# Performance work log

Measured on AMD Instinct MI355X. Metric: run time of the kernel, lower is better.

## Reference

```python
import jax, jax.numpy as jnp
import numpy as np

N_PTS = 20000  # points per cloud


def setup_inputs() -> dict:
    key = jax.random.key(0)
    k1, k2 = jax.random.split(key)
    preds = jax.random.normal(k1, (N_PTS, 3), dtype=jnp.float32)
    gts = jax.random.normal(k2, (1, N_PTS, 3), dtype=jnp.float32)
    return {"preds": preds, "gts": gts}


def reference(preds, gts):
    # x = gts: [B, Nx, 3]; y = preds.unsqueeze(0): [1, Ny, 3] (B must be 1 for bmm)
    y = preds[None]                                   # [1, Ny, 3]
    x = gts                                           # [1, Nx, 3]
    xx = jnp.sum(x * x, axis=-1)                      # [1, Nx]  (diag of x x^T)
    yy = jnp.sum(y * y, axis=-1)                      # [1, Ny]
    zz = jnp.einsum('bnd,bmd->bnm', x, y)             # [1, Nx, Ny]
    P = xx[:, :, None] + yy[:, None, :] - 2.0 * zz    # [1, Nx, Ny] squared dists
    dist1 = jnp.min(P, axis=1)                        # [1, Ny] min over gts points
    dist2 = jnp.min(P, axis=2)                        # [1, Nx] min over pred points
    idx1 = jnp.argmin(P, axis=1)                      # [1, Ny]
    idx2 = jnp.argmin(P, axis=2)                      # [1, Nx]
    return dist1, dist2, idx1, idx2
```

## Files before the change

kernel.cpp:

```cpp
#include <hip/hip_runtime.h>

#define N_PTS  20000
#define NG     128
#define NC     (NG * NG)
#define GMIN   (-6.0f)
#define GINV   (NG / 12.0f)
#define MARGIN 5e-4f
#define SSTRIDE (N_PTS / 64)
#define QB79   79

__device__ __forceinline__ float np_self_dot(float x, float y, float z) {
    return __fadd_rn(__fadd_rn(__fmul_rn(x, x), __fmul_rn(y, y)),
                     __fmul_rn(z, z));
}
__device__ __forceinline__ unsigned ordmap(float f) {
    unsigned b = __float_as_uint(f);
    return (b & 0x80000000u) ? ~b : (b | 0x80000000u);
}
__device__ __forceinline__ float invord(unsigned h) {
    return __uint_as_float((h & 0x80000000u) ? (h ^ 0x80000000u) : ~h);
}
__device__ __forceinline__ int cellC(float v) {
    int c = (int)((v - GMIN) * GINV);
    return c < 0 ? 0 : (c > NG - 1 ? NG - 1 : c);
}
__device__ __forceinline__ unsigned long long wave_min_u64(unsigned long long k) {
    #pragma unroll
    for (int m = 1; m < 64; m <<= 1) {
        unsigned long long o = __shfl_xor(k, m, 64);
        k = (o < k) ? o : k;
    }
    return k;
}

__global__ __launch_bounds__(256) void k_hist(
    const float* __restrict__ preds, const float* __restrict__ gts,
    int* __restrict__ cursor)
{
    int t = blockIdx.x * 256 + threadIdx.x;
    if (t >= 2 * N_PTS) return;
    int cl = t / N_PTS, i = t - cl * N_PTS;
    const float* src = cl ? gts : preds;
    int cell = cellC(src[i*3+0]) * NG + cellC(src[i*3+1]);
    atomicAdd(&cursor[cl * NC + cell], 1);
}

__global__ __launch_bounds__(1024) void k_scan(
    int* __restrict__ cursor, int* __restrict__ bstart)
{
    __shared__ int wsum[16];
    __shared__ int wpre[16];
    int cl = blockIdx.x, t = threadIdx.x;
    int wave = t >> 6, lane = t & 63;

    int base = cl * NC + t * 16;
    const int4* c4 = (const int4*)(cursor + base);
    int4 a = c4[0], b = c4[1], c = c4[2], d = c4[3];
    int v[16] = { a.x, a.y, a.z, a.w, b.x, b.y, b.z, b.w,
                  c.x, c.y, c.z, c.w, d.x, d.y, d.z, d.w };
    int s = 0;
    #pragma unroll
    for (int i = 0; i < 16; ++i) s += v[i];

    int ps = s;
    #pragma unroll
    for (int m = 1; m < 64; m <<= 1) {
        int o = __shfl_up(ps, m, 64);
        if (lane >= m) ps += o;
    }
    if (lane == 63) wsum[wave] = ps;
    __syncthreads();
    if (t < 16) {
        int x = wsum[t];
        int px = x;
        #pragma unroll
        for (int m = 1; m < 16; m <<= 1) {
            int o = __shfl_up(px, m, 16);
            if ((t & 15) >= m) px += o;
        }
        wpre[t] = px - x;
    }
    __syncthreads();

    int run = wpre[wave] + (ps - s);
    #pragma unroll
    for (int i = 0; i < 16; ++i) {
        bstart[cl * (NC + 1) + t * 16 + i] = run;
        cursor[base + i] = run;
        run += v[i];
    }
    if (t == 1023) bstart[cl * (NC + 1) + NC] = run;
}

__global__ __launch_bounds__(256) void k_scatter(
    const float* __restrict__ preds, const float* __restrict__ gts,
    int* __restrict__ cursor, float4* __restrict__ sorted)
{
    int t = blockIdx.x * 256 + threadIdx.x;
    if (t >= 2 * N_PTS) return;
    int cl = t / N_PTS, i = t - cl * N_PTS;
    const float* src = cl ? gts : preds;
    float x = src[i*3+0], y = src[i*3+1], z = src[i*3+2];
    int cell = cellC(x) * NG + cellC(y);
    int pos = atomicAdd(&cursor[cl * NC + cell], 1);
    sorted[(size_t)cl * N_PTS + pos] = make_float4(x, y, z, __int_as_float(i));
}

__global__ __launch_bounds__(64) void k_main(
    const float4* __restrict__ sorted, const int* __restrict__ bstart,
    float* __restrict__ out)
{
    int wid  = blockIdx.x;
    int lane = threadIdx.x;
    int dir  = wid / N_PTS;
    int qpos = wid - dir * N_PTS;
    int rcl  = 1 - dir;

    const float4* rs = sorted + (size_t)rcl * N_PTS;
    const int*    cs = bstart + rcl * (NC + 1);

    float4 samp = rs[lane * SSTRIDE];
    float4 qv   = sorted[(size_t)dir * N_PTS + qpos];
    int    origq = __float_as_int(qv.w);
    float qx = qv.x, qy = qv.y, qz = qv.z;
    float sq = np_self_dot(qx, qy, qz);

    unsigned long long key = ~0ULL;

#define EVAL(r)                                                            \
    {   float sr = np_self_dot((r).x, (r).y, (r).z);                       \
        float zz = __fadd_rn(__fadd_rn(__fmul_rn(qx, (r).x),               \
                                       __fmul_rn(qy, (r).y)),              \
                             __fmul_rn(qz, (r).z));                        \
        float P  = __fsub_rn(__fadd_rn(sq, sr), __fadd_rn(zz, zz));        \
        unsigned long long kk =                                            \
            ((unsigned long long)ordmap(P) << 32) | __float_as_uint((r).w);\
        key = (kk < key) ? kk : key; }

#define STREAM(LO, HI)                                                     \
    {   int p = (LO) + lane;                                               \
        for (; p + 192 < (HI); p += 256) {                                 \
            float4 r0 = rs[p],       r1 = rs[p + 64];                      \
            float4 r2 = rs[p + 128], r3 = rs[p + 192];                     \
            EVAL(r0) EVAL(r1) EVAL(r2) EVAL(r3)                            \
        }                                                                  \
        for (; p + 64 < (HI); p += 128) {                                  \
            float4 r0 = rs[p], r1 = rs[p + 64];                            \
            EVAL(r0) EVAL(r1)                                              \
        }                                                                  \
        if (p < (HI)) { float4 r0 = rs[p]; EVAL(r0) }                      \
    }

    int cx = cellC(qx), cy = cellC(qy);
    int sxL = cx > 0 ? cx - 1 : 0, sxR = cx < NG-1 ? cx + 1 : NG-1;
    int syL = cy > 0 ? cy - 1 : 0, syR = cy < NG-1 ? cy + 1 : NG-1;
    int slo = cs[sxL * NG + syL];
    int shi = cs[sxR * NG + syR + 1];
    STREAM(slo, shi)
    EVAL(samp)

    key = wave_min_u64(key);
    float W = sqrtf(invord((unsigned)(key >> 32)) + MARGIN);
    int txL = cellC(qx - W), txR = cellC(qx + W);
    int tyL = cellC(qy - W), tyR = cellC(qy + W);
    int lo2 = cs[txL * NG + tyL];
    int hi2 = cs[txR * NG + tyR + 1];
    if (lo2 < slo) STREAM(lo2, slo)
    if (hi2 > shi) STREAM(shi, hi2)
    key = wave_min_u64(key);
#undef STREAM
#undef EVAL

    if (lane == 0) {
        out[dir * N_PTS + origq]       = invord((unsigned)(key >> 32));
        out[(2 + dir) * N_PTS + origq] = (float)(unsigned)(key & 0xFFFFFFFFu);
    }
}

__device__ __forceinline__ float np_pair(float sq, float sr,
                                         float qx, float qy, float qz,
                                         float rx, float ry, float rz) {
    float zz = __fadd_rn(__fadd_rn(__fmul_rn(qx, rx), __fmul_rn(qy, ry)),
                         __fmul_rn(qz, rz));
    return __fsub_rn(__fadd_rn(sq, sr), __fadd_rn(zz, zz));
}

__global__ __launch_bounds__(256) void chamfer_direct_kernel(
    const float* __restrict__ preds, const float* __restrict__ gts,
    float* __restrict__ out)
{
    __shared__ float4 spts[256];
    int bid = blockIdx.x;
    int dir = bid / QB79;
    int qb  = bid - dir * QB79;
    int q   = qb * 256 + threadIdx.x;

    const float* qpts = (dir == 0) ? preds : gts;
    const float* rpts = (dir == 0) ? gts   : preds;

    int qc = (q < N_PTS) ? q : (N_PTS - 1);
    float qx = qpts[qc*3+0], qy = qpts[qc*3+1], qz = qpts[qc*3+2];
    float sq = np_self_dot(qx, qy, qz);
    float best = 3.4e38f;
    int   bidx = 0;

    for (int t = 0; t < N_PTS; t += 256) {
        int cnt = min(256, N_PTS - t);
        __syncthreads();
        if ((int)threadIdx.x < cnt) {
            int j = t + threadIdx.x;
            float rx = rpts[j*3+0], ry = rpts[j*3+1], rz = rpts[j*3+2];
            spts[threadIdx.x] = make_float4(rx, ry, rz, np_self_dot(rx, ry, rz));
        }
        __syncthreads();
        for (int k = 0; k < cnt; ++k) {
            float4 r = spts[k];
            float d = np_pair(sq, r.w, qx, qy, qz, r.x, r.y, r.z);
            if (d < best) { best = d; bidx = t + k; }
        }
    }
    if (q < N_PTS) {
        out[dir * N_PTS + q]       = best;
        out[(2 + dir) * N_PTS + q] = (float)bidx;
    }
}

extern "C" void kernel_launch(void* const* d_in, const int* in_sizes, int n_in,
                              void* d_out, int out_size, void* d_ws, size_t ws_size,
                              hipStream_t stream) {
    const float* preds = (const float*)d_in[0];
    const float* gts   = (const float*)d_in[1];
    float* out = (float*)d_out;

    char* w = (char*)d_ws;
    size_t sorted_b = (size_t)2 * N_PTS * sizeof(float4);
    size_t bstart_b = (size_t)2 * (NC + 1) * sizeof(int);
    size_t cursor_b = (size_t)2 * NC * sizeof(int);
    size_t need = sorted_b + bstart_b + cursor_b;

    if (ws_size >= need) {
        float4* sorted = (float4*)w;
        int* bstart = (int*)(w + sorted_b);
        int* cursor = (int*)(w + sorted_b + bstart_b);

        hipMemsetAsync(cursor, 0, cursor_b, stream);
        k_hist<<<(2 * N_PTS + 255) / 256, 256, 0, stream>>>(preds, gts, cursor);
        k_scan<<<2, 1024, 0, stream>>>(cursor, bstart);
        k_scatter<<<(2 * N_PTS + 255) / 256, 256, 0, stream>>>(
            preds, gts, cursor, sorted);
        k_main<<<2 * N_PTS, 64, 0, stream>>>(sorted, bstart, out);
    } else {
        chamfer_direct_kernel<<<2 * QB79, 256, 0, stream>>>(preds, gts, out);
    }
}
```

Baseline: 126.6 us.

## Stream only per-row cell spans in grid NN search instead of contiguous ranges

The nearest-neighbor query now loads per-x-row cell boundaries in parallel across lanes and streams only the y-window span within each row, instead of scanning the whole contiguous sorted range from the first to the last cell. The second pass is skipped when the search window already lies inside the initial 3x3 neighborhood, and otherwise re-scans the full window row by row. A software-prefetched single-element loop flattens the three row spans so the lanes stay busy. This is meant to cut the many irrelevant points evaluated between rows, at the cost of extra shuffles, index arithmetic and re-evaluating points already covered by the first pass.

```diff
diff --git a/kernel.cpp b/kernel.cpp
--- a/kernel.cpp
+++ b/kernel.cpp
@@ -31,6 +31,37 @@
         k = (o < k) ? o : k;
     }
     return k;
+}
+
+#define EVAL(r)                                                            \
+    {   float sr = np_self_dot((r).x, (r).y, (r).z);                       \
+        float zz = __fadd_rn(__fadd_rn(__fmul_rn(qx, (r).x),               \
+                                       __fmul_rn(qy, (r).y)),              \
+                             __fmul_rn(qz, (r).z));                        \
+        float P  = __fsub_rn(__fadd_rn(sq, sr), __fadd_rn(zz, zz));        \
+        unsigned long long kk =                                            \
+            ((unsigned long long)ordmap(P) << 32) | __float_as_uint((r).w);\
+        key = (kk < key) ? kk : key; }
+
+__device__ __forceinline__ void stream3(
+    const float4* __restrict__ rs, int lane,
+    int lo0, int c0, int lo1, int c1, int lo2, int c2,
+    float qx, float qy, float qz, float sq, unsigned long long& key)
+{
+    int s01 = c0 + c1, tot = s01 + c2;
+    int t = lane;
+    if (t < tot) {
+        int p = t < c0 ? lo0 + t : t < s01 ? lo1 + (t - c0) : lo2 + (t - s01);
+        float4 rc = rs[p];
+        for (t += 64; t < tot; t += 64) {
+            int pn = t < c0 ? lo0 + t : t < s01 ? lo1 + (t - c0)
+                                                : lo2 + (t - s01);
+            float4 rn = rs[pn];
+            EVAL(rc)
+            rc = rn;
+        }
+        EVAL(rc)
+    }
 }
 
 __global__ __launch_bounds__(256) void k_hist(
@@ -126,50 +157,50 @@
     float sq = np_self_dot(qx, qy, qz);
 
     unsigned long long key = ~0ULL;
-
-#define EVAL(r)                                                            \
-    {   float sr = np_self_dot((r).x, (r).y, (r).z);                       \
-        float zz = __fadd_rn(__fadd_rn(__fmul_rn(qx, (r).x),               \
-                                       __fmul_rn(qy, (r).y)),              \
-                             __fmul_rn(qz, (r).z));                        \
-        float P  = __fsub_rn(__fadd_rn(sq, sr), __fadd_rn(zz, zz));        \
-        unsigned long long kk =                                            \
-            ((unsigned long long)ordmap(P) << 32) | __float_as_uint((r).w);\
-        key = (kk < key) ? kk : key; }
-
-#define STREAM(LO, HI)                                                     \
-    {   int p = (LO) + lane;                                               \
-        for (; p + 192 < (HI); p += 256) {                                 \
-            float4 r0 = rs[p],       r1 = rs[p + 64];                      \
-            float4 r2 = rs[p + 128], r3 = rs[p + 192];                     \
-            EVAL(r0) EVAL(r1) EVAL(r2) EVAL(r3)                            \
-        }                                                                  \
-        for (; p + 64 < (HI); p += 128) {                                  \
-            float4 r0 = rs[p], r1 = rs[p + 64];                            \
-            EVAL(r0) EVAL(r1)                                              \
-        }                                                                  \
-        if (p < (HI)) { float4 r0 = rs[p]; EVAL(r0) }                      \
-    }
+    int l31 = lane & 31;
 
     int cx = cellC(qx), cy = cellC(qy);
     int sxL = cx > 0 ? cx - 1 : 0, sxR = cx < NG-1 ? cx + 1 : NG-1;
     int syL = cy > 0 ? cy - 1 : 0, syR = cy < NG-1 ? cy + 1 : NG-1;
-    int slo = cs[sxL * NG + syL];
-    int shi = cs[sxR * NG + syR + 1];
-    STREAM(slo, shi)
+    int nrs  = sxR - sxL + 1;
+    int xrS  = sxL + (l31 < nrs ? l31 : nrs - 1);
+    int colS = (lane < 32) ? syL : (syR + 1);
+    int bndS = cs[xrS * NG + colS];
+    int lo0 = __shfl(bndS, 0, 64), hi0 = __shfl(bndS, 32, 64);
+    int lo1 = __shfl(bndS, 1, 64), hi1 = __shfl(bndS, 33, 64);
+    int lo2 = __shfl(bndS, 2, 64), hi2 = __shfl(bndS, 34, 64);
+    int c0 = hi0 - lo0;
+    int c1 = nrs > 1 ? hi1 - lo1 : 0;
+    int c2 = nrs > 2 ? hi2 - lo2 : 0;
+    stream3(rs, lane, lo0, c0, lo1, c1, lo2, c2, qx, qy, qz, sq, key);
     EVAL(samp)
 
     key = wave_min_u64(key);
     float W = sqrtf(invord((unsigned)(key >> 32)) + MARGIN);
     int txL = cellC(qx - W), txR = cellC(qx + W);
     int tyL = cellC(qy - W), tyR = cellC(qy + W);
-    int lo2 = cs[txL * NG + tyL];
-    int hi2 = cs[txR * NG + tyR + 1];
-    if (lo2 < slo) STREAM(lo2, slo)
-    if (hi2 > shi) STREAM(shi, hi2)
-    key = wave_min_u64(key);
-#undef STREAM
-#undef EVAL
+    if (!(txL >= sxL && txR <= sxR && tyL >= syL && tyR <= syR)) {
+        int R = txR - txL + 1;
+        for (int g = 0; g < R; g += 32) {
+            int rows = R - g; if (rows > 32) rows = 32;
+            int xr2  = txL + g + (l31 < rows ? l31 : rows - 1);
+            int col2 = (lane < 32) ? tyL : (tyR + 1);
+            int b2 = cs[xr2 * NG + col2];
+            for (int r0 = 0; r0 < rows; r0 += 3) {
+                int i1 = r0 + 1 < rows ? r0 + 1 : rows - 1;
+                int i2 = r0 + 2 < rows ? r0 + 2 : rows - 1;
+                int L0 = __shfl(b2, r0, 64), H0 = __shfl(b2, 32 + r0, 64);
+                int L1 = __shfl(b2, i1, 64), H1 = __shfl(b2, 32 + i1, 64);
+                int L2 = __shfl(b2, i2, 64), H2 = __shfl(b2, 32 + i2, 64);
+                int d0 = H0 - L0;
+                int d1 = (r0 + 1 < rows) ? H1 - L1 : 0;
+                int d2 = (r0 + 2 < rows) ? H2 - L2 : 0;
+                stream3(rs, lane, L0, d0, L1, d1, L2, d2,
+                        qx, qy, qz, sq, key);
+            }
+        }
+        key = wave_min_u64(key);
+    }
 
     if (lane == 0) {
         out[dir * N_PTS + origq]       = invord((unsigned)(key >> 32));
```

New measurement: 122.4 us. 3.3% less time.

## Process two queries per wave and scan exact cell rectangles per row

Applied to the files above, without the earlier changes.

Each wave now handles two adjacent sorted query points and shares every loaded reference point between them, halving the block count. Instead of streaming the contiguous range from the first to last cell (which spans whole x-rows of the grid), it reads per-row segment bounds for the exact cell rectangle and packs three rows at a time across lanes. The second pass is skipped when the refined window lies inside the first rectangle. In exchange, the union rectangle for two queries can be larger than either query needs, and the per-row bookkeeping adds shuffles and index arithmetic.

```diff
diff --git a/kernel.cpp b/kernel.cpp
--- a/kernel.cpp
+++ b/kernel.cpp
@@ -32,6 +32,27 @@
     }
     return k;
 }
+__device__ __forceinline__ int imin2(int a, int b) { return a < b ? a : b; }
+__device__ __forceinline__ int imax2(int a, int b) { return a > b ? a : b; }
+
+#define EVAL2(r)                                                           \
+    {   float rx = (r).x, ry = (r).y, rz = (r).z;                          \
+        float sr = np_self_dot(rx, ry, rz);                                \
+        unsigned ridx = __float_as_uint((r).w);                            \
+        float za = __fadd_rn(__fadd_rn(__fmul_rn(qax, rx),                 \
+                                       __fmul_rn(qay, ry)),                \
+                             __fmul_rn(qaz, rz));                          \
+        float Pa = __fsub_rn(__fadd_rn(sqa, sr), __fadd_rn(za, za));       \
+        unsigned long long kka =                                           \
+            ((unsigned long long)ordmap(Pa) << 32) | ridx;                 \
+        ka = (kka < ka) ? kka : ka;                                        \
+        float zb = __fadd_rn(__fadd_rn(__fmul_rn(qbx, rx),                 \
+                                       __fmul_rn(qby, ry)),                \
+                             __fmul_rn(qbz, rz));                          \
+        float Pb = __fsub_rn(__fadd_rn(sqb, sr), __fadd_rn(zb, zb));       \
+        unsigned long long kkb =                                           \
+            ((unsigned long long)ordmap(Pb) << 32) | ridx;                 \
+        kb = (kkb < kb) ? kkb : kb; }
 
 __global__ __launch_bounds__(256) void k_hist(
     const float* __restrict__ preds, const float* __restrict__ gts,
@@ -112,68 +133,90 @@
 {
     int wid  = blockIdx.x;
     int lane = threadIdx.x;
-    int dir  = wid / N_PTS;
-    int qpos = wid - dir * N_PTS;
+    int q0   = wid * 2;
+    int dir  = q0 / N_PTS;
+    int qp0  = q0 - dir * N_PTS;
     int rcl  = 1 - dir;
 
     const float4* rs = sorted + (size_t)rcl * N_PTS;
     const int*    cs = bstart + rcl * (NC + 1);
 
     float4 samp = rs[lane * SSTRIDE];
-    float4 qv   = sorted[(size_t)dir * N_PTS + qpos];
-    int    origq = __float_as_int(qv.w);
-    float qx = qv.x, qy = qv.y, qz = qv.z;
-    float sq = np_self_dot(qx, qy, qz);
-
-    unsigned long long key = ~0ULL;
-
-#define EVAL(r)                                                            \
-    {   float sr = np_self_dot((r).x, (r).y, (r).z);                       \
-        float zz = __fadd_rn(__fadd_rn(__fmul_rn(qx, (r).x),               \
-                                       __fmul_rn(qy, (r).y)),              \
-                             __fmul_rn(qz, (r).z));                        \
-        float P  = __fsub_rn(__fadd_rn(sq, sr), __fadd_rn(zz, zz));        \
-        unsigned long long kk =                                            \
-            ((unsigned long long)ordmap(P) << 32) | __float_as_uint((r).w);\
-        key = (kk < key) ? kk : key; }
-
-#define STREAM(LO, HI)                                                     \
-    {   int p = (LO) + lane;                                               \
-        for (; p + 192 < (HI); p += 256) {                                 \
-            float4 r0 = rs[p],       r1 = rs[p + 64];                      \
-            float4 r2 = rs[p + 128], r3 = rs[p + 192];                     \
-            EVAL(r0) EVAL(r1) EVAL(r2) EVAL(r3)                            \
+    float4 qva  = sorted[(size_t)dir * N_PTS + qp0];
+    float4 qvb  = sorted[(size_t)dir * N_PTS + qp0 + 1];
+    int oa = __float_as_int(qva.w), ob = __float_as_int(qvb.w);
+    float qax = qva.x, qay = qva.y, qaz = qva.z;
+    float qbx = qvb.x, qby = qvb.y, qbz = qvb.z;
+    float sqa = np_self_dot(qax, qay, qaz);
+    float sqb = np_self_dot(qbx, qby, qbz);
+
+    unsigned long long ka = ~0ULL, kb = ~0ULL;
+    int l31 = lane & 31;
+
+#define SCAN_RECT(xL, xR, yL, yR)                                          \
+    {   int R = (xR) - (xL) + 1;                                           \
+        for (int g = 0; g < R; g += 32) {                                  \
+            int rows = R - g; if (rows > 32) rows = 32;                    \
+            int xr  = (xL) + g + (l31 < rows ? l31 : rows - 1);            \
+            int col = (lane < 32) ? (yL) : ((yR) + 1);                     \
+            int b2 = cs[xr * NG + col];                                    \
+            for (int r0 = 0; r0 < rows; r0 += 3) {                         \
+                int i1 = r0 + 1 < rows ? r0 + 1 : rows - 1;                \
+                int i2 = r0 + 2 < rows ? r0 + 2 : rows - 1;                \
+                int L0 = __shfl(b2, r0, 64), H0 = __shfl(b2, 32 + r0, 64); \
+                int L1 = __shfl(b2, i1, 64), H1 = __shfl(b2, 32 + i1, 64); \
+                int L2 = __shfl(b2, i2, 64), H2 = __shfl(b2, 32 + i2, 64); \
+                int d0 = H0 - L0;                                          \
+                int d1 = (r0 + 1 < rows) ? H1 - L1 : 0;                    \
+                int d2 = (r0 + 2 < rows) ? H2 - L2 : 0;                    \
+                int s01 = d0 + d1, tot = s01 + d2;                         \
+                int t = lane;                                              \
+                if (t < tot) {                                             \
+                    int p = t < d0 ? L0 + t : t < s01 ? L1 + (t - d0)      \
+                                                      : L2 + (t - s01);   \
+                    float4 rc = rs[p];                                     \
+                    for (t += 64; t < tot; t += 64) {                      \
+                        int pn = t < d0 ? L0 + t : t < s01 ? L1 + (t - d0) \
+                                                           : L2 + (t - s01);\
+                        float4 rn = rs[pn];                                \
+                        EVAL2(rc)                                          \
+                        rc = rn;                                           \
+                    }                                                      \
+                    EVAL2(rc)                                              \
+                }                                                          \
+            }                                                              \
         }                                                                  \
-        for (; p + 64 < (HI); p += 128) {                                  \
-            float4 r0 = rs[p], r1 = rs[p + 64];                            \
-            EVAL(r0) EVAL(r1)                                              \
-        }                                                                  \
-        if (p < (HI)) { float4 r0 = rs[p]; EVAL(r0) }                      \
-    }
-
-    int cx = cellC(qx), cy = cellC(qy);
-    int sxL = cx > 0 ? cx - 1 : 0, sxR = cx < NG-1 ? cx + 1 : NG-1;
-    int syL = cy > 0 ? cy - 1 : 0, syR = cy < NG-1 ? cy + 1 : NG-1;
-    int slo = cs[sxL * NG + syL];
-    int shi = cs[sxR * NG + syR + 1];
-    STREAM(slo, shi)
-    EVAL(samp)
-
-    key = wave_min_u64(key);
-    float W = sqrtf(invord((unsigned)(key >> 32)) + MARGIN);
-    int txL = cellC(qx - W), txR = cellC(qx + W);
-    int tyL = cellC(qy - W), tyR = cellC(qy + W);
-    int lo2 = cs[txL * NG + tyL];
-    int hi2 = cs[txR * NG + tyR + 1];
-    if (lo2 < slo) STREAM(lo2, slo)
-    if (hi2 > shi) STREAM(shi, hi2)
-    key = wave_min_u64(key);
-#undef STREAM
-#undef EVAL
+    }
+
+    int cxa = cellC(qax), cya = cellC(qay);
+    int cxb = cellC(qbx), cyb = cellC(qby);
+    int sxL = imax2(imin2(cxa, cxb) - 1, 0);
+    int sxR = imin2(imax2(cxa, cxb) + 1, NG - 1);
+    int syL = imax2(imin2(cya, cyb) - 1, 0);
+    int syR = imin2(imax2(cya, cyb) + 1, NG - 1);
+    SCAN_RECT(sxL, sxR, syL, syR)
+    EVAL2(samp)
+
+    ka = wave_min_u64(ka);
+    kb = wave_min_u64(kb);
+    float Wa = sqrtf(invord((unsigned)(ka >> 32)) + MARGIN);
+    float Wb = sqrtf(invord((unsigned)(kb >> 32)) + MARGIN);
+    int txL = imin2(cellC(qax - Wa), cellC(qbx - Wb));
+    int txR = imax2(cellC(qax + Wa), cellC(qbx + Wb));
+    int tyL = imin2(cellC(qay - Wa), cellC(qby - Wb));
+    int tyR = imax2(cellC(qay + Wa), cellC(qby + Wb));
+    if (!(txL >= sxL && txR <= sxR && tyL >= syL && tyR <= syR)) {
+        SCAN_RECT(txL, txR, tyL, tyR)
+        ka = wave_min_u64(ka);
+        kb = wave_min_u64(kb);
+    }
+#undef SCAN_RECT
 
     if (lane == 0) {
-        out[dir * N_PTS + origq]       = invord((unsigned)(key >> 32));
-        out[(2 + dir) * N_PTS + origq] = (float)(unsigned)(key & 0xFFFFFFFFu);
+        out[dir * N_PTS + oa]       = invord((unsigned)(ka >> 32));
+        out[(2 + dir) * N_PTS + oa] = (float)(unsigned)(ka & 0xFFFFFFFFu);
+        out[dir * N_PTS + ob]       = invord((unsigned)(kb >> 32));
+        out[(2 + dir) * N_PTS + ob] = (float)(unsigned)(kb & 0xFFFFFFFFu);
     }
 }
 
@@ -248,7 +291,7 @@
         k_scan<<<2, 1024, 0, stream>>>(cursor, bstart);
         k_scatter<<<(2 * N_PTS + 255) / 256, 256, 0, stream>>>(
             preds, gts, cursor, sorted);
-        k_main<<<2 * N_PTS, 64, 0, stream>>>(sorted, bstart, out);
+        k_main<<<N_PTS, 64, 0, stream>>>(sorted, bstart, out);
     } else {
         chamfer_direct_kernel<<<2 * QB79, 256, 0, stream>>>(preds, gts, out);
     }
```

Result: slower. 135.8 us (+7.3%).

## Scan grid rectangles row-by-row instead of contiguous index range

Applied to the files above, without the earlier changes.

Replaces streaming the whole contiguous sorted-index span (which covers entire rows of cells between the corner cells) with a per-row rectangle scan that fetches row start and end offsets via shuffles and processes three rows per batch. The initial search window grows from 3x3 to 5x5 cells, and the second pass is skipped when the refined window fits inside the first rectangle. This is meant to cut the many wasted point evaluations from full-row spans, in exchange for more index arithmetic, shuffles and a possibly rescanned overlap in the second pass.

```diff
diff --git a/kernel.cpp b/kernel.cpp
--- a/kernel.cpp
+++ b/kernel.cpp
@@ -32,6 +32,16 @@
     }
     return k;
 }
+
+#define EVAL(r)                                                            \
+    {   float sr = np_self_dot((r).x, (r).y, (r).z);                       \
+        float zz = __fadd_rn(__fadd_rn(__fmul_rn(qx, (r).x),               \
+                                       __fmul_rn(qy, (r).y)),              \
+                             __fmul_rn(qz, (r).z));                        \
+        float P  = __fsub_rn(__fadd_rn(sq, sr), __fadd_rn(zz, zz));        \
+        unsigned long long kk =                                            \
+            ((unsigned long long)ordmap(P) << 32) | __float_as_uint((r).w);\
+        key = (kk < key) ? kk : key; }
 
 __global__ __launch_bounds__(256) void k_hist(
     const float* __restrict__ preds, const float* __restrict__ gts,
@@ -126,50 +136,58 @@
     float sq = np_self_dot(qx, qy, qz);
 
     unsigned long long key = ~0ULL;
-
-#define EVAL(r)                                                            \
-    {   float sr = np_self_dot((r).x, (r).y, (r).z);                       \
-        float zz = __fadd_rn(__fadd_rn(__fmul_rn(qx, (r).x),               \
-                                       __fmul_rn(qy, (r).y)),              \
-                             __fmul_rn(qz, (r).z));                        \
-        float P  = __fsub_rn(__fadd_rn(sq, sr), __fadd_rn(zz, zz));        \
-        unsigned long long kk =                                            \
-            ((unsigned long long)ordmap(P) << 32) | __float_as_uint((r).w);\
-        key = (kk < key) ? kk : key; }
-
-#define STREAM(LO, HI)                                                     \
-    {   int p = (LO) + lane;                                               \
-        for (; p + 192 < (HI); p += 256) {                                 \
-            float4 r0 = rs[p],       r1 = rs[p + 64];                      \
-            float4 r2 = rs[p + 128], r3 = rs[p + 192];                     \
-            EVAL(r0) EVAL(r1) EVAL(r2) EVAL(r3)                            \
+    int l31 = lane & 31;
+
+#define SCAN_RECT(xL, xR, yL, yR)                                          \
+    {   int R = (xR) - (xL) + 1;                                           \
+        for (int g = 0; g < R; g += 32) {                                  \
+            int rows = R - g; if (rows > 32) rows = 32;                    \
+            int xr  = (xL) + g + (l31 < rows ? l31 : rows - 1);            \
+            int col = (lane < 32) ? (yL) : ((yR) + 1);                     \
+            int b2 = cs[xr * NG + col];                                    \
+            for (int r0 = 0; r0 < rows; r0 += 3) {                         \
+                int i1 = r0 + 1 < rows ? r0 + 1 : rows - 1;                \
+                int i2 = r0 + 2 < rows ? r0 + 2 : rows - 1;                \
+                int L0 = __shfl(b2, r0, 64), H0 = __shfl(b2, 32 + r0, 64); \
+                int L1 = __shfl(b2, i1, 64), H1 = __shfl(b2, 32 + i1, 64); \
+                int L2 = __shfl(b2, i2, 64), H2 = __shfl(b2, 32 + i2, 64); \
+                int d0 = H0 - L0;                                          \
+                int d1 = (r0 + 1 < rows) ? H1 - L1 : 0;                    \
+                int d2 = (r0 + 2 < rows) ? H2 - L2 : 0;                    \
+                int s01 = d0 + d1, tot = s01 + d2;                         \
+                int t = lane;                                              \
+                if (t < tot) {                                             \
+                    int p = t < d0 ? L0 + t : t < s01 ? L1 + (t - d0)      \
+                                                      : L2 + (t - s01);   \
+                    float4 rc = rs[p];                                     \
+                    for (t += 64; t < tot; t += 64) {                      \
+                        int pn = t < d0 ? L0 + t : t < s01 ? L1 + (t - d0) \
+                                                           : L2 + (t - s01);\
+                        float4 rn = rs[pn];                                \
+                        EVAL(rc)                                           \
+                        rc = rn;                                           \
+                    }                                                      \
+                    EVAL(rc)                                               \
+                }                                                          \
+            }                                                              \
         }                                                                  \
-        for (; p + 64 < (HI); p += 128) {                                  \
-            float4 r0 = rs[p], r1 = rs[p + 64];                            \
-            EVAL(r0) EVAL(r1)                                              \
-        }                                                                  \
-        if (p < (HI)) { float4 r0 = rs[p]; EVAL(r0) }                      \
     }
 
     int cx = cellC(qx), cy = cellC(qy);
-    int sxL = cx > 0 ? cx - 1 : 0, sxR = cx < NG-1 ? cx + 1 : NG-1;
-    int syL = cy > 0 ? cy - 1 : 0, syR = cy < NG-1 ? cy + 1 : NG-1;
-    int slo = cs[sxL * NG + syL];
-    int shi = cs[sxR * NG + syR + 1];
-    STREAM(slo, shi)
+    int sxL = cx > 1 ? cx - 2 : 0, sxR = cx < NG-2 ? cx + 2 : NG-1;
+    int syL = cy > 1 ? cy - 2 : 0, syR = cy < NG-2 ? cy + 2 : NG-1;
+    SCAN_RECT(sxL, sxR, syL, syR)
     EVAL(samp)
 
     key = wave_min_u64(key);
     float W = sqrtf(invord((unsigned)(key >> 32)) + MARGIN);
     int txL = cellC(qx - W), txR = cellC(qx + W);
     int tyL = cellC(qy - W), tyR = cellC(qy + W);
-    int lo2 = cs[txL * NG + tyL];
-    int hi2 = cs[txR * NG + tyR + 1];
-    if (lo2 < slo) STREAM(lo2, slo)
-    if (hi2 > shi) STREAM(shi, hi2)
-    key = wave_min_u64(key);
-#undef STREAM
-#undef EVAL
+    if (!(txL >= sxL && txR <= sxR && tyL >= syL && tyR <= syR)) {
+        SCAN_RECT(txL, txR, tyL, tyR)
+        key = wave_min_u64(key);
+    }
+#undef SCAN_RECT
 
     if (lane == 0) {
         out[dir * N_PTS + origq]       = invord((unsigned)(key >> 32));
```

Measured after the change: 119.8 us. 5.3% less time.
